# Performance work log

Hardware: AMD Instinct MI355X
Metric: run time of the kernel (lower is better)

## Reference

```python
import jax, jax.numpy as jnp
import numpy as np
import math

B, N, D = 64, 512, 1024
SHELL_DIM, RFF_DIM, ORDER = 64, 32, 4
CHARGE_COUPLING, SHELL_COUPLING = 1.0, 0.5
DIST_COUPLING, DIST_SCALE = 0.3, 10.0
COMBINED_DIM = 64


def setup_inputs() -> dict:
    key = jax.random.key(0)
    ks = jax.random.split(key, 12)
    s = 0.02
    inp = {
        "x": jax.random.normal(ks[0], (B, N, D), dtype=jnp.float32),
        "W_charge": jax.random.normal(ks[1], (1, D), dtype=jnp.float32) * s,
        "b_charge": jnp.zeros((1,), dtype=jnp.float32),
        "W_shell": jax.random.normal(ks[2], (SHELL_DIM, D), dtype=jnp.float32) * s,
        "b_shell": jnp.zeros((SHELL_DIM,), dtype=jnp.float32),
        # RFF params (learnable=True in source): omega ~ N(0,1)*sqrt(coupling), bias ~ U(0, 2pi)
        "omega": jax.random.normal(ks[3], (RFF_DIM, SHELL_DIM), dtype=jnp.float32) * math.sqrt(SHELL_COUPLING),
        "rff_bias": jax.random.uniform(ks[4], (RFF_DIM,), dtype=jnp.float32) * (2.0 * math.pi),
        "W_combine": jax.random.normal(ks[5], (COMBINED_DIM, (ORDER + 1) * 2 * RFF_DIM), dtype=jnp.float32) * s,
        "W_v": jax.random.normal(ks[6], (D, D), dtype=jnp.float32) * s,
        "b_v": jnp.zeros((D,), dtype=jnp.float32),
        "W_out": jax.random.normal(ks[7], (D, D), dtype=jnp.float32) * s,
        "b_out": jnp.zeros((D,), dtype=jnp.float32),
        "log_temp": jnp.zeros((), dtype=jnp.float32),
    }
    return inp


def _forward(x, W_charge, b_charge, W_shell, b_shell, omega, rff_bias,
             W_combine, W_v, b_v, W_out, b_out, log_temp):
    b, n, d = x.shape
    # charge: (B,N) in [-1,1]
    q = jnp.tanh(x @ W_charge.T + b_charge)[..., 0]
    # polynomial charge features: sqrt(|(-k)^n/n!| + 1e-10) * q^n, n=0..ORDER
    coeffs = jnp.asarray([(-CHARGE_COUPLING) ** m / math.factorial(m) for m in range(ORDER + 1)], dtype=x.dtype)
    mags = jnp.sqrt(jnp.abs(coeffs) + 1e-10)  # (5,)
    phi_c = mags * q[..., None] ** jnp.arange(ORDER + 1)  # (B,N,5)
    # shell: normalized linear projection
    shell = x @ W_shell.T + b_shell
    shell = shell / jnp.maximum(jnp.linalg.norm(shell, axis=-1, keepdims=True), 1e-12)
    # random Fourier features
    proj = shell @ omega.T + rff_bias  # (B,N,RFF)
    rff_scale = math.sqrt(2.0 / (2 * RFF_DIM)) * math.sqrt(math.exp(-SHELL_COUPLING))
    phi_s = jnp.concatenate([jnp.cos(proj), jnp.sin(proj)], axis=-1) * rff_scale  # (B,N,64)
    # tensor product -> combine projection (no bias)
    tp = (phi_c[..., :, None] * phi_s[..., None, :]).reshape(b, n, -1)  # (B,N,5*64)
    phi = tp @ W_combine.T  # (B,N,64)
    # Toeplitz distance weighting exp(-coupling*|i-j|/scale)
    idx = jnp.arange(n)
    T = jnp.exp(-DIST_COUPLING * jnp.abs(idx[:, None] - idx[None, :]).astype(x.dtype) / DIST_SCALE)
    temp = jax.nn.softplus(log_temp) + 0.1
    logits = jnp.einsum('bnd,bmd->bnm', phi, phi) * T / temp
    # causal mask (allow j <= i)
    causal = idx[:, None] >= idx[None, :]
    logits = jnp.where(causal, logits, -jnp.inf)
    attn = jax.nn.softmax(logits, axis=-1)
    V = x @ W_v.T + b_v
    out = jnp.einsum('bnm,bmd->bnd', attn, V)
    return out @ W_out.T + b_out


def reference(x, W_charge, b_charge, W_shell, b_shell, omega, rff_bias,
              W_combine, W_v, b_v, W_out, b_out, log_temp):
    return _forward(x, W_charge, b_charge, W_shell, b_shell, omega, rff_bias,
                    W_combine, W_v, b_v, W_out, b_out, log_temp)
```

## Files before the change

### kernel.cpp

```cpp
#include <hip/hip_runtime.h>
#include <hip/hip_bf16.h>
#include <math.h>


using u16 = unsigned short;
typedef short short8 __attribute__((ext_vector_type(8)));
typedef float f32x4 __attribute__((ext_vector_type(4)));

__device__ __forceinline__ u16 f2bf(float f) {
  unsigned u = __float_as_uint(f);
  return (u16)((u + 0x7fffu + ((u >> 16) & 1u)) >> 16);
}

__device__ __forceinline__ void gload16(const u16* g, const u16* l) {
  __builtin_amdgcn_global_load_lds(
      (const __attribute__((address_space(1))) unsigned int*)(g),
      (__attribute__((address_space(3))) unsigned int*)(l),
      16, 0, 0);
}

__device__ __forceinline__ short8 ldsrd(const u16* base, int row, int b) {
  int byte = row * 128 + (b ^ ((row & 7) << 4));
  return *reinterpret_cast<const short8*>(reinterpret_cast<const char*>(base) + byte);
}

__global__ __launch_bounds__(256) void convert_x_kernel(const float* __restrict__ in,
                                                        u16* __restrict__ out, int n4) {
  int idx = blockIdx.x * 256 + threadIdx.x;
  int stride = gridDim.x * 256;
  for (int i = idx; i < n4; i += stride) {
    float4 v = reinterpret_cast<const float4*>(in)[i];
    ushort4 o;
    o.x = f2bf(v.x); o.y = f2bf(v.y); o.z = f2bf(v.z); o.w = f2bf(v.w);
    reinterpret_cast<ushort4*>(out)[i] = o;
  }
}

__global__ __launch_bounds__(256) void prep_weights_kernel(
    const float* __restrict__ Wv, const float* __restrict__ Wo,
    const float* __restrict__ Wsh, const float* __restrict__ Wch,
    const float* __restrict__ Wcb,
    u16* __restrict__ wvb, u16* __restrict__ wob,
    u16* __restrict__ wcat, u16* __restrict__ wcbb) {
  int i = blockIdx.x * 256 + threadIdx.x;
  if (i < 1048576) { wvb[i] = f2bf(Wv[i]); return; }
  i -= 1048576;
  if (i < 1048576) { wob[i] = f2bf(Wo[i]); return; }
  i -= 1048576;
  if (i < 131072) {
    int row = i >> 10, e = i & 1023;
    float v = (row < 64) ? Wsh[i] : ((row == 64) ? Wch[e] : 0.0f);
    wcat[i] = f2bf(v);
    return;
  }
  i -= 131072;
  if (i < 40960) {
    int row = i / 320;
    wcbb[i] = f2bf(row < 64 ? Wcb[i] : 0.0f);
  }
}

template<int OUT_MODE>
__global__ __launch_bounds__(512, 2) void gemm256(
    const u16* __restrict__ A, const u16* __restrict__ Bt,
    const float* __restrict__ bias, void* __restrict__ Cv,
    int M, int N, int K, int lda, int ldb, int ldc,
    long long sA, long long sB, long long sC) {
  (void)M; (void)N;
  __shared__ u16 lds[65536];
  const int t = threadIdx.x;
  const int lane = t & 63;
  const int w = t >> 6;
  const u16* Ag = A + (size_t)blockIdx.z * sA;
  const u16* Bg = Bt + (size_t)blockIdx.z * sB;

  int gx = gridDim.x, gy = gridDim.y;
  int bid = blockIdx.y * gx + blockIdx.x;
  int nwg = gx * gy;
  if ((nwg & 7) == 0) { int cpx = nwg >> 3; bid = (bid & 7) * cpx + (bid >> 3); }
  const int m0 = (bid / gx) * 256;
  const int n0 = (bid % gx) * 256;

  const int wm = w >> 2;
  const int wn = w & 3;
  const int rl = lane & 15;
  const int kq = lane >> 4;

  const int srow = w * 8 + (lane >> 3);
  const int scol = 8 * ((lane & 7) ^ ((lane >> 3) & 7));
  const u16* aS = Ag + (size_t)(m0 + srow) * lda + scol;
  const u16* bS = Bg + (size_t)(n0 + srow) * ldb + scol;

  const int NT = K >> 6;

  #pragma unroll
  for (int g = 0; g < 4; ++g) {
    gload16(aS + (size_t)(g * 64) * lda, lds + w * 512 + g * 4096);
    gload16(bS + (size_t)(g * 64) * ldb, lds + 16384 + w * 512 + g * 4096);
  }

  f32x4 acc[8][4] = {};

  for (int tt = 0; tt < NT; ++tt) {
    const int c = tt & 1, nc = c ^ 1;
    const u16* At  = lds + c * 32768;
    const u16* Btl = At + 16384;
    const u16* dA  = lds + nc * 32768 + w * 512;
    const u16* dB  = dA + 16384;
    const int kn = (tt + 1 < NT ? tt + 1 : 0) << 6;

    __builtin_amdgcn_s_barrier();
    #pragma unroll
    for (int g = 0; g < 4; ++g) {
      gload16(aS + (size_t)(g * 64) * lda + kn, dA + g * 4096);
      gload16(bS + (size_t)(g * 64) * ldb + kn, dB + g * 4096);
    }
    asm volatile("s_waitcnt vmcnt(8)" ::: "memory");
    __builtin_amdgcn_s_barrier();
    __builtin_amdgcn_sched_barrier(0);

    short8 bq[4][2];
    #pragma unroll
    for (int p = 0; p < 4; ++p) {
      if (p == 0) {
        #pragma unroll
        for (int ni = 0; ni < 4; ++ni)
          #pragma unroll
          for (int ks = 0; ks < 2; ++ks)
            bq[ni][ks] = ldsrd(Btl, wn * 64 + ni * 16 + rl, ks * 64 + kq * 16);
      }
      short8 a0k0 = ldsrd(At, wm * 128 + (2 * p + 0) * 16 + rl, 0 + kq * 16);
      short8 a0k1 = ldsrd(At, wm * 128 + (2 * p + 0) * 16 + rl, 64 + kq * 16);
      short8 a1k0 = ldsrd(At, wm * 128 + (2 * p + 1) * 16 + rl, 0 + kq * 16);
      short8 a1k1 = ldsrd(At, wm * 128 + (2 * p + 1) * 16 + rl, 64 + kq * 16);
      __builtin_amdgcn_s_setprio(1);
      #pragma unroll
      for (int ni = 0; ni < 4; ++ni) {
        acc[2 * p][ni]     = __builtin_amdgcn_mfma_f32_16x16x32_bf16(a0k0, bq[ni][0], acc[2 * p][ni], 0, 0, 0);
        acc[2 * p][ni]     = __builtin_amdgcn_mfma_f32_16x16x32_bf16(a0k1, bq[ni][1], acc[2 * p][ni], 0, 0, 0);
        acc[2 * p + 1][ni] = __builtin_amdgcn_mfma_f32_16x16x32_bf16(a1k0, bq[ni][0], acc[2 * p + 1][ni], 0, 0, 0);
        acc[2 * p + 1][ni] = __builtin_amdgcn_mfma_f32_16x16x32_bf16(a1k1, bq[ni][1], acc[2 * p + 1][ni], 0, 0, 0);
      }
      __builtin_amdgcn_s_setprio(0);
    }
  }

  const int cm = (lane >> 4) * 4;
  #pragma unroll
  for (int mi = 0; mi < 8; ++mi) {
    #pragma unroll
    for (int ni = 0; ni < 4; ++ni) {
      const int gm = m0 + wm * 128 + mi * 16 + cm;
      const int gn = n0 + wn * 64 + ni * 16 + rl;
      const float bsv = bias ? bias[gn] : 0.0f;
      if (OUT_MODE == 0) {
        float* C = (float*)Cv + (size_t)blockIdx.z * sC;
        #pragma unroll
        for (int r = 0; r < 4; ++r)
          C[(size_t)(gm + r) * ldc + gn] = acc[mi][ni][r] + bsv;
      } else if (OUT_MODE == 1) {
        u16* C = (u16*)Cv + (size_t)blockIdx.z * sC;
        #pragma unroll
        for (int r = 0; r < 4; ++r)
          C[(size_t)(gm + r) * ldc + gn] = f2bf(acc[mi][ni][r] + bsv);
      } else {
        u16* C = (u16*)Cv + (size_t)blockIdx.z * sC;
        ushort4 pk;
        pk.x = f2bf(acc[mi][ni][0] + bsv);
        pk.y = f2bf(acc[mi][ni][1] + bsv);
        pk.z = f2bf(acc[mi][ni][2] + bsv);
        pk.w = f2bf(acc[mi][ni][3] + bsv);
        *reinterpret_cast<ushort4*>(&C[(size_t)gn * ldc + gm]) = pk;
      }
    }
  }
}

template<int OUT_MODE>
__global__ __launch_bounds__(256) void gemm_bt(
    const u16* __restrict__ A, const u16* __restrict__ Bt,
    const float* __restrict__ bias, void* __restrict__ Cv,
    int M, int N, int K, int lda, int ldb, int ldc,
    long long sA, long long sB, long long sC) {
  (void)M; (void)N;
  __shared__ u16 lA[128 * 32];
  __shared__ u16 lB[128 * 32];
  const int t = threadIdx.x;
  const int lane = t & 63;
  const int w = t >> 6;
  const u16* Ag = A + (size_t)blockIdx.z * sA;
  const u16* Bg = Bt + (size_t)blockIdx.z * sB;

  int gx = gridDim.x, gy = gridDim.y;
  int bid = blockIdx.y * gx + blockIdx.x;
  int nwg = gx * gy;
  if ((nwg & 7) == 0) { int cpx = nwg >> 3; bid = (bid & 7) * cpx + (bid >> 3); }
  const int m0 = (bid / gx) * 128;
  const int n0 = (bid % gx) * 128;

  const int wm = (w >> 1) * 64;
  const int wn = (w & 1) * 64;
  const int rl = lane & 15;
  const int kl = (lane >> 4) * 8;
  const int rs = w * 32 + (lane >> 2);
  const int cs = (lane & 3) * 8;
  u16* ldsA = &lA[w * 1024];
  u16* ldsB = &lB[w * 1024];

  f32x4 acc[4][4] = {};

  for (int k0 = 0; k0 < K; k0 += 32) {
    const u16* ga = Ag + (size_t)(m0 + rs) * lda + k0 + cs;
    const u16* gb = Bg + (size_t)(n0 + rs) * ldb + k0 + cs;
    gload16(ga,                    ldsA);
    gload16(ga + (size_t)16 * lda, ldsA + 512);
    gload16(gb,                    ldsB);
    gload16(gb + (size_t)16 * ldb, ldsB + 512);
    __syncthreads();
    short8 af[4], bfr[4];
    #pragma unroll
    for (int mi = 0; mi < 4; ++mi)
      af[mi] = *reinterpret_cast<const short8*>(&lA[(wm + mi * 16 + rl) * 32 + kl]);
    #pragma unroll
    for (int ni = 0; ni < 4; ++ni)
      bfr[ni] = *reinterpret_cast<const short8*>(&lB[(wn + ni * 16 + rl) * 32 + kl]);
    #pragma unroll
    for (int mi = 0; mi < 4; ++mi) {
      #pragma unroll
      for (int ni = 0; ni < 4; ++ni)
        acc[mi][ni] = __builtin_amdgcn_mfma_f32_16x16x32_bf16(af[mi], bfr[ni], acc[mi][ni], 0, 0, 0);
    }
    __syncthreads();
  }

  const int cm = (lane >> 4) * 4;
  #pragma unroll
  for (int mi = 0; mi < 4; ++mi) {
    #pragma unroll
    for (int ni = 0; ni < 4; ++ni) {
      const int gm = m0 + wm + mi * 16 + cm;
      const int gn = n0 + wn + ni * 16 + rl;
      const float bsv = bias ? bias[gn] : 0.0f;
      if (OUT_MODE == 0) {
        float* C = (float*)Cv + (size_t)blockIdx.z * sC;
        #pragma unroll
        for (int r = 0; r < 4; ++r)
          C[(size_t)(gm + r) * ldc + gn] = acc[mi][ni][r] + bsv;
      } else if (OUT_MODE == 1) {
        u16* C = (u16*)Cv + (size_t)blockIdx.z * sC;
        #pragma unroll
        for (int r = 0; r < 4; ++r)
          C[(size_t)(gm + r) * ldc + gn] = f2bf(acc[mi][ni][r] + bsv);
      } else {
        u16* C = (u16*)Cv + (size_t)blockIdx.z * sC;
        ushort4 pk;
        pk.x = f2bf(acc[mi][ni][0] + bsv);
        pk.y = f2bf(acc[mi][ni][1] + bsv);
        pk.z = f2bf(acc[mi][ni][2] + bsv);
        pk.w = f2bf(acc[mi][ni][3] + bsv);
        *reinterpret_cast<ushort4*>(&C[(size_t)gn * ldc + gm]) = pk;
      }
    }
  }
}

__global__ __launch_bounds__(256) void features_kernel(
    const float* __restrict__ SC, const float* __restrict__ b_shell,
    const float* __restrict__ b_charge, const float* __restrict__ omega,
    const float* __restrict__ rff_bias, u16* __restrict__ tp) {
  __shared__ __align__(16) float sm[4][64];
  const int lane = threadIdx.x & 63;
  const int w = threadIdx.x >> 6;
  const int row = blockIdx.x * 4 + w;
  const float* sc = SC + (size_t)row * 128;
  float s = sc[lane] + b_shell[lane];
  float ss = s * s;
  #pragma unroll
  for (int off = 32; off > 0; off >>= 1) ss += __shfl_xor(ss, off);
  float shell = s / fmaxf(sqrtf(ss), 1e-12f);
  sm[w][lane] = shell;
  const float q = tanhf(sc[64] + b_charge[0]);
  __syncthreads();
  const int r = lane & 31;
  float p = rff_bias[r];
  const float4* om = reinterpret_cast<const float4*>(omega + r * 64);
  const float4* sv = reinterpret_cast<const float4*>(sm[w]);
  #pragma unroll
  for (int d = 0; d < 16; ++d) {
    float4 o4 = om[d], s4 = sv[d];
    p += o4.x * s4.x + o4.y * s4.y + o4.z * s4.z + o4.w * s4.w;
  }
  const float RFFS = 0.13767388f;
  float phis = (lane < 32) ? cosf(p) * RFFS : sinf(p) * RFFS;
  float q2 = q * q;
  float pc[5];
  pc[0] = 1.0f;
  pc[1] = q;
  pc[2] = 0.70710678f * q2;
  pc[3] = 0.40824829f * q2 * q;
  pc[4] = 0.20412415f * q2 * q2;
  u16* o = tp + (size_t)row * 320 + lane;
  #pragma unroll
  for (int m = 0; m < 5; ++m) o[m * 64] = f2bf(pc[m] * phis);
}

__global__ __launch_bounds__(256) void softmax_kernel(
    const float* __restrict__ logits, const float* __restrict__ log_temp,
    u16* __restrict__ attn) {
  __shared__ float rb[8];
  const int rowid = blockIdx.x;
  const int i = rowid & 511;
  const float* L = logits + (size_t)rowid * 512;
  u16* Ar = attn + (size_t)rowid * 512;
  const int t = threadIdx.x, lane = t & 63, w = t >> 6;
  const float invt = 1.0f / (log1pf(expf(log_temp[0])) + 0.1f);
  const int j0 = t, j1 = t + 256;
  float z0 = (j0 <= i) ? L[j0] * expf(-0.03f * (float)(i - j0)) * invt : -INFINITY;
  float z1 = (j1 <= i) ? L[j1] * expf(-0.03f * (float)(i - j1)) * invt : -INFINITY;
  float m = fmaxf(z0, z1);
  #pragma unroll
  for (int off = 32; off > 0; off >>= 1) m = fmaxf(m, __shfl_xor(m, off));
  if (lane == 0) rb[w] = m;
  __syncthreads();
  m = fmaxf(fmaxf(rb[0], rb[1]), fmaxf(rb[2], rb[3]));
  float e0 = expf(z0 - m);
  float e1 = expf(z1 - m);
  float sum = e0 + e1;
  #pragma unroll
  for (int off = 32; off > 0; off >>= 1) sum += __shfl_xor(sum, off);
  if (lane == 0) rb[4 + w] = sum;
  __syncthreads();
  const float inv = 1.0f / (rb[4] + rb[5] + rb[6] + rb[7]);
  Ar[j0] = f2bf(e0 * inv);
  Ar[j1] = f2bf(e1 * inv);
}

extern "C" void kernel_launch(void* const* d_in, const int* in_sizes, int n_in,
                              void* d_out, int out_size, void* d_ws, size_t ws_size,
                              hipStream_t stream) {
  (void)in_sizes; (void)n_in; (void)out_size; (void)ws_size;
  const float* x     = (const float*)d_in[0];
  const float* Wch   = (const float*)d_in[1];
  const float* bch   = (const float*)d_in[2];
  const float* Wsh   = (const float*)d_in[3];
  const float* bsh   = (const float*)d_in[4];
  const float* omega = (const float*)d_in[5];
  const float* rffb  = (const float*)d_in[6];
  const float* Wcb   = (const float*)d_in[7];
  const float* Wv    = (const float*)d_in[8];
  const float* bv    = (const float*)d_in[9];
  const float* Wo    = (const float*)d_in[10];
  const float* bo    = (const float*)d_in[11];
  const float* lt    = (const float*)d_in[12];
  float* out = (float*)d_out;
  char* ws = (char*)d_ws;

  u16*   xb   = (u16*)(ws + 0);
  u16*   vt   = (u16*)(ws + 67108864);
  float* sc   = (float*)(ws + 67108864);
  u16*   attn = (u16*)(ws + 134217728);
  u16*   tp   = (u16*)(ws + 134217728);
  u16*   phi  = (u16*)(ws + 167772160);
  u16*   wvb  = (u16*)(ws + 176160768);
  u16*   wob  = (u16*)(ws + 178257920);
  u16*   wcat = (u16*)(ws + 180355072);
  u16*   wcbb = (u16*)(ws + 180617216);
  float* logits = out;
  u16*   out2 = xb;

  convert_x_kernel<<<8192, 256, 0, stream>>>(x, xb, 33554432 / 4);
  prep_weights_kernel<<<8864, 256, 0, stream>>>(Wv, Wo, Wsh, Wch, Wcb, wvb, wob, wcat, wcbb);
  gemm_bt<0><<<dim3(1, 256, 1), 256, 0, stream>>>(xb, wcat, nullptr, sc,
      32768, 128, 1024, 1024, 1024, 128, 0, 0, 0);
  features_kernel<<<8192, 256, 0, stream>>>(sc, bsh, bch, omega, rffb, tp);
  gemm_bt<1><<<dim3(1, 256, 1), 256, 0, stream>>>(tp, wcbb, nullptr, phi,
      32768, 128, 320, 320, 320, 128, 0, 0, 0);
  gemm_bt<0><<<dim3(4, 4, 64), 256, 0, stream>>>(phi, phi, nullptr, logits,
      512, 512, 64, 128, 128, 512, 65536, 65536, 262144);
  softmax_kernel<<<32768, 256, 0, stream>>>(logits, lt, attn);
  gemm256<2><<<dim3(4, 128, 1), 512, 0, stream>>>(xb, wvb, bv, vt,
      32768, 1024, 1024, 1024, 1024, 32768, 0, 0, 0);
  gemm256<1><<<dim3(4, 2, 64), 512, 0, stream>>>(attn, vt, nullptr, out2,
      512, 1024, 512, 512, 32768, 1024, 262144, 512, 524288);
  gemm256<0><<<dim3(4, 128, 1), 512, 0, stream>>>(out2, wob, bo, out,
      32768, 1024, 1024, 1024, 1024, 1024, 0, 0, 0);
}
```

Measured before the change: 635.2 us.

## Fuse QK logits GEMM into softmax and interleave prefetch loads in gemm256

Replaces the separate phi·phi^T GEMM and softmax with one kernel. It stages all 512 key rows of a batch in LDS, computes a 64-row logits tile with MFMA in registers, and applies the distance decay, causal mask and softmax directly before writing bf16 attention. This removes the round trip of the float32 logits tensor through global memory and one launch. Separately, the gemm256 main loop now spreads its global-to-LDS prefetches across the compute phases. B is prefetched two tiles ahead into the buffer just consumed, and extra barriers are added per phase. That trades more synchronisation for better overlap of loads with MFMA work.

```diff
diff --git a/kernel.cpp b/kernel.cpp
--- a/kernel.cpp
+++ b/kernel.cpp
@@ -94,10 +94,14 @@
   const int NT = K >> 6;
 
   #pragma unroll
-  for (int g = 0; g < 4; ++g) {
-    gload16(aS + (size_t)(g * 64) * lda, lds + w * 512 + g * 4096);
-    gload16(bS + (size_t)(g * 64) * ldb, lds + 16384 + w * 512 + g * 4096);
-  }
+  for (int g = 0; g < 4; ++g)
+    gload16(aS + (size_t)(g * 64) * lda,      lds + w * 512 + g * 4096);
+  #pragma unroll
+  for (int g = 0; g < 4; ++g)
+    gload16(bS + (size_t)(g * 64) * ldb,      lds + 16384 + w * 512 + g * 4096);
+  #pragma unroll
+  for (int g = 0; g < 4; ++g)
+    gload16(bS + (size_t)(g * 64) * ldb + 64, lds + 32768 + 16384 + w * 512 + g * 4096);
 
   f32x4 acc[8][4] = {};
 
@@ -105,17 +109,12 @@
     const int c = tt & 1, nc = c ^ 1;
     const u16* At  = lds + c * 32768;
     const u16* Btl = At + 16384;
-    const u16* dA  = lds + nc * 32768 + w * 512;
-    const u16* dB  = dA + 16384;
-    const int kn = (tt + 1 < NT ? tt + 1 : 0) << 6;
-
-    __builtin_amdgcn_s_barrier();
-    #pragma unroll
-    for (int g = 0; g < 4; ++g) {
-      gload16(aS + (size_t)(g * 64) * lda + kn, dA + g * 4096);
-      gload16(bS + (size_t)(g * 64) * ldb + kn, dB + g * 4096);
-    }
-    asm volatile("s_waitcnt vmcnt(8)" ::: "memory");
+    const u16* dstA = lds + nc * 32768 + w * 512;
+    const u16* dstB = lds + c * 32768 + 16384 + w * 512;
+    const int kA = (tt + 1 < NT) ? (tt + 1) << 6 : 0;
+    const int kB = (tt + 2 < NT) ? (tt + 2) << 6 : 0;
+
+    asm volatile("s_waitcnt vmcnt(4)" ::: "memory");
     __builtin_amdgcn_s_barrier();
     __builtin_amdgcn_sched_barrier(0);
 
@@ -124,15 +123,23 @@
     for (int p = 0; p < 4; ++p) {
       if (p == 0) {
         #pragma unroll
-        for (int ni = 0; ni < 4; ++ni)
-          #pragma unroll
-          for (int ks = 0; ks < 2; ++ks)
-            bq[ni][ks] = ldsrd(Btl, wn * 64 + ni * 16 + rl, ks * 64 + kq * 16);
+        for (int ni = 0; ni < 4; ++ni) {
+          bq[ni][0] = ldsrd(Btl, wn * 64 + ni * 16 + rl, kq * 16);
+          bq[ni][1] = ldsrd(Btl, wn * 64 + ni * 16 + rl, 64 + kq * 16);
+        }
       }
-      short8 a0k0 = ldsrd(At, wm * 128 + (2 * p + 0) * 16 + rl, 0 + kq * 16);
+      short8 a0k0 = ldsrd(At, wm * 128 + (2 * p + 0) * 16 + rl, kq * 16);
       short8 a0k1 = ldsrd(At, wm * 128 + (2 * p + 0) * 16 + rl, 64 + kq * 16);
-      short8 a1k0 = ldsrd(At, wm * 128 + (2 * p + 1) * 16 + rl, 0 + kq * 16);
+      short8 a1k0 = ldsrd(At, wm * 128 + (2 * p + 1) * 16 + rl, kq * 16);
       short8 a1k1 = ldsrd(At, wm * 128 + (2 * p + 1) * 16 + rl, 64 + kq * 16);
+      if (p < 2) {
+        gload16(aS + (size_t)((2 * p + 0) * 64) * lda + kA, dstA + (2 * p + 0) * 4096);
+        gload16(aS + (size_t)((2 * p + 1) * 64) * lda + kA, dstA + (2 * p + 1) * 4096);
+      } else {
+        gload16(bS + (size_t)((2 * (p - 2) + 0) * 64) * ldb + kB, dstB + (2 * (p - 2) + 0) * 4096);
+        gload16(bS + (size_t)((2 * (p - 2) + 1) * 64) * ldb + kB, dstB + (2 * (p - 2) + 1) * 4096);
+      }
+      __builtin_amdgcn_s_barrier();
       __builtin_amdgcn_s_setprio(1);
       #pragma unroll
       for (int ni = 0; ni < 4; ++ni) {
@@ -142,8 +149,11 @@
         acc[2 * p + 1][ni] = __builtin_amdgcn_mfma_f32_16x16x32_bf16(a1k1, bq[ni][1], acc[2 * p + 1][ni], 0, 0, 0);
       }
       __builtin_amdgcn_s_setprio(0);
+      __builtin_amdgcn_s_barrier();
     }
   }
+
+  asm volatile("s_waitcnt vmcnt(0)" ::: "memory");
 
   const int cm = (lane >> 4) * 4;
   #pragma unroll
@@ -246,19 +256,11 @@
         #pragma unroll
         for (int r = 0; r < 4; ++r)
           C[(size_t)(gm + r) * ldc + gn] = acc[mi][ni][r] + bsv;
-      } else if (OUT_MODE == 1) {
+      } else {
         u16* C = (u16*)Cv + (size_t)blockIdx.z * sC;
         #pragma unroll
         for (int r = 0; r < 4; ++r)
           C[(size_t)(gm + r) * ldc + gn] = f2bf(acc[mi][ni][r] + bsv);
-      } else {
-        u16* C = (u16*)Cv + (size_t)blockIdx.z * sC;
-        ushort4 pk;
-        pk.x = f2bf(acc[mi][ni][0] + bsv);
-        pk.y = f2bf(acc[mi][ni][1] + bsv);
-        pk.z = f2bf(acc[mi][ni][2] + bsv);
-        pk.w = f2bf(acc[mi][ni][3] + bsv);
-        *reinterpret_cast<ushort4*>(&C[(size_t)gn * ldc + gm]) = pk;
       }
     }
   }
@@ -304,35 +306,75 @@
   for (int m = 0; m < 5; ++m) o[m * 64] = f2bf(pc[m] * phis);
 }
 
-__global__ __launch_bounds__(256) void softmax_kernel(
-    const float* __restrict__ logits, const float* __restrict__ log_temp,
+__global__ __launch_bounds__(256, 2) void qk_softmax_kernel(
+    const u16* __restrict__ phi, const float* __restrict__ log_temp,
     u16* __restrict__ attn) {
-  __shared__ float rb[8];
-  const int rowid = blockIdx.x;
-  const int i = rowid & 511;
-  const float* L = logits + (size_t)rowid * 512;
-  u16* Ar = attn + (size_t)rowid * 512;
-  const int t = threadIdx.x, lane = t & 63, w = t >> 6;
+  __shared__ u16 sm[36864];
+  const int t = threadIdx.x;
+  const int lane = t & 63;
+  const int w = t >> 6;
+  const int b = blockIdx.y;
+  const int rt = blockIdx.x;
+  const u16* phiB = phi + (size_t)b * 512 * 128;
+
+  const int srow = w * 8 + (lane >> 3);
+  const int scol = 8 * ((lane & 7) ^ ((lane >> 3) & 7));
+  #pragma unroll
+  for (int rnd = 0; rnd < 16; ++rnd)
+    gload16(phiB + (size_t)(rnd * 32 + srow) * 128 + scol, sm + rnd * 2048 + w * 512);
+  #pragma unroll
+  for (int rnd = 0; rnd < 2; ++rnd)
+    gload16(phiB + (size_t)(rt * 64 + rnd * 32 + srow) * 128 + scol,
+            sm + 32768 + rnd * 2048 + w * 512);
+  __syncthreads();
+
+  const u16* Kb = sm;
+  const u16* Qb = sm + 32768;
+  const int rl = lane & 15;
+  const int kq = lane >> 4;
+
+  short8 af0 = ldsrd(Qb, w * 16 + rl, kq * 16);
+  short8 af1 = ldsrd(Qb, w * 16 + rl, 64 + kq * 16);
+  f32x4 acc[32] = {};
+  #pragma unroll
+  for (int cf = 0; cf < 32; ++cf) {
+    short8 b0 = ldsrd(Kb, cf * 16 + rl, kq * 16);
+    short8 b1 = ldsrd(Kb, cf * 16 + rl, 64 + kq * 16);
+    acc[cf] = __builtin_amdgcn_mfma_f32_16x16x32_bf16(af0, b0, acc[cf], 0, 0, 0);
+    acc[cf] = __builtin_amdgcn_mfma_f32_16x16x32_bf16(af1, b1, acc[cf], 0, 0, 0);
+  }
+
   const float invt = 1.0f / (log1pf(expf(log_temp[0])) + 0.1f);
-  const int j0 = t, j1 = t + 256;
-  float z0 = (j0 <= i) ? L[j0] * expf(-0.03f * (float)(i - j0)) * invt : -INFINITY;
-  float z1 = (j1 <= i) ? L[j1] * expf(-0.03f * (float)(i - j1)) * invt : -INFINITY;
-  float m = fmaxf(z0, z1);
-  #pragma unroll
-  for (int off = 32; off > 0; off >>= 1) m = fmaxf(m, __shfl_xor(m, off));
-  if (lane == 0) rb[w] = m;
-  __syncthreads();
-  m = fmaxf(fmaxf(rb[0], rb[1]), fmaxf(rb[2], rb[3]));
-  float e0 = expf(z0 - m);
-  float e1 = expf(z1 - m);
-  float sum = e0 + e1;
-  #pragma unroll
-  for (int off = 32; off > 0; off >>= 1) sum += __shfl_xor(sum, off);
-  if (lane == 0) rb[4 + w] = sum;
-  __syncthreads();
-  const float inv = 1.0f / (rb[4] + rb[5] + rb[6] + rb[7]);
-  Ar[j0] = f2bf(e0 * inv);
-  Ar[j1] = f2bf(e1 * inv);
+  float tj[32];
+  #pragma unroll
+  for (int cf = 0; cf < 32; ++cf) tj[cf] = expf(0.03f * (float)(cf * 16 + rl));
+
+  u16* Ar = attn + ((size_t)b * 512 + rt * 64 + w * 16 + (lane >> 4) * 4) * 512 + rl;
+  #pragma unroll
+  for (int r = 0; r < 4; ++r) {
+    const int i = rt * 64 + w * 16 + (lane >> 4) * 4 + r;
+    const float ti = expf(-0.03f * (float)i) * invt;
+    float z[32];
+    #pragma unroll
+    for (int cf = 0; cf < 32; ++cf) {
+      const int j = cf * 16 + rl;
+      z[cf] = (j <= i) ? acc[cf][r] * tj[cf] * ti : -INFINITY;
+    }
+    float m = z[0];
+    #pragma unroll
+    for (int cf = 1; cf < 32; ++cf) m = fmaxf(m, z[cf]);
+    #pragma unroll
+    for (int off = 8; off > 0; off >>= 1) m = fmaxf(m, __shfl_xor(m, off));
+    float sum = 0.0f;
+    #pragma unroll
+    for (int cf = 0; cf < 32; ++cf) { z[cf] = expf(z[cf] - m); sum += z[cf]; }
+    #pragma unroll
+    for (int off = 8; off > 0; off >>= 1) sum += __shfl_xor(sum, off);
+    const float rinv = 1.0f / sum;
+    #pragma unroll
+    for (int cf = 0; cf < 32; ++cf)
+      Ar[(size_t)r * 512 + cf * 16] = f2bf(z[cf] * rinv);
+  }
 }
 
 extern "C" void kernel_launch(void* const* d_in, const int* in_sizes, int n_in,
@@ -365,7 +407,6 @@
   u16*   wob  = (u16*)(ws + 178257920);
   u16*   wcat = (u16*)(ws + 180355072);
   u16*   wcbb = (u16*)(ws + 180617216);
-  float* logits = out;
   u16*   out2 = xb;
 
   convert_x_kernel<<<8192, 256, 0, stream>>>(x, xb, 33554432 / 4);
@@ -375,9 +416,7 @@
   features_kernel<<<8192, 256, 0, stream>>>(sc, bsh, bch, omega, rffb, tp);
   gemm_bt<1><<<dim3(1, 256, 1), 256, 0, stream>>>(tp, wcbb, nullptr, phi,
       32768, 128, 320, 320, 320, 128, 0, 0, 0);
-  gemm_bt<0><<<dim3(4, 4, 64), 256, 0, stream>>>(phi, phi, nullptr, logits,
-      512, 512, 64, 128, 128, 512, 65536, 65536, 262144);
-  softmax_kernel<<<32768, 256, 0, stream>>>(logits, lt, attn);
+  qk_softmax_kernel<<<dim3(8, 64), 256, 0, stream>>>(phi, lt, attn);
   gemm256<2><<<dim3(4, 128, 1), 512, 0, stream>>>(xb, wvb, bv, vt,
       32768, 1024, 1024, 1024, 1024, 32768, 0, 0, 0);
   gemm256<1><<<dim3(4, 2, 64), 512, 0, stream>>>(attn, vt, nullptr, out2,
```

Result: faster. 579.8 us (-8.7%).
